# Kernel tuning notes

Hardware: AMD Instinct MI355X
Metric: run time of the kernel (lower is better)

The kernel has to match this reference:

```python
import jax, jax.numpy as jnp
import numpy as np

CON_SIZE = 1024  # num_gz; used in the 1/sqrt(con_size) score scaling


def setup_inputs() -> dict:
    key = jax.random.key(0)
    k1, k2, k3, k4, k5 = jax.random.split(key, 5)
    B, K, D, P = 1024, 256, 1024, 768
    return {
        "joint_feature": jax.random.normal(k1, (B, D), dtype=jnp.float32),
        "confounder_dictionary": jax.random.normal(k2, (K, D), dtype=jnp.float32),
        "prior": jax.random.uniform(k3, (K, 1), dtype=jnp.float32),
        "Wq": jax.random.normal(k4, (D, P), dtype=jnp.float32) * (1.0 / np.sqrt(D)),
        "Wk": jax.random.normal(k5, (D, P), dtype=jnp.float32) * (1.0 / np.sqrt(D)),
    }


def reference(joint_feature, confounder_dictionary, prior, Wq, Wk):
    # dot_product_intervention
    q = joint_feature @ Wq                       # [B, 768]
    k = confounder_dictionary @ Wk               # [K, 768]
    scores = (q @ k.T) * (1.0 / jnp.sqrt(jnp.float32(CON_SIZE)))  # [B, K]
    attn = jax.nn.softmax(scores, axis=-1)       # softmax over confounders
    # (attn[b,k,1] * conf[k,d] * prior[k,1]).sum(1)  == attn @ (conf * prior)
    g_z = jnp.einsum('bk,kd->bd', attn, confounder_dictionary * prior)  # [B, D]
    return joint_feature + g_z
```

## Files before the change

### kernel.cpp

```cpp
#include <hip/hip_runtime.h>
#include <hip/hip_bf16.h>


typedef __attribute__((ext_vector_type(8))) short short8;
typedef __attribute__((ext_vector_type(4))) float f32x4;

__device__ __forceinline__ ushort f2bf(float x) {
    union { float f; uint u; } c; c.f = x;
    return (ushort)((c.u + 0x7FFFu + ((c.u >> 16) & 1u)) >> 16);
}
__device__ __forceinline__ float bflo(uint u) {
    union { uint u; float f; } c; c.u = u << 16; return c.f;
}
__device__ __forceinline__ float bfhi(uint u) {
    union { uint u; float f; } c; c.u = u & 0xFFFF0000u; return c.f;
}

__global__ __launch_bounds__(256)
void prep_kernel(const float* __restrict__ J, const float* __restrict__ conf,
                 const float* __restrict__ prior, const float* __restrict__ Wq,
                 const float* __restrict__ Wk,
                 ushort* __restrict__ Jb, ushort* __restrict__ confb,
                 ushort* __restrict__ WqT, ushort* __restrict__ WkT,
                 ushort* __restrict__ cpT)
{
    const int t = threadIdx.x;
    int b = blockIdx.x;

    if (b < 1280) {
        const float* src; ushort* dst; int base;
        if (b < 1024) { src = J;    dst = Jb;    base = b * 1024; }
        else          { src = conf; dst = confb; base = (b - 1024) * 1024; }
        const float4 v = *(const float4*)(src + base + t * 4);
        ushort4 o;
        o.x = f2bf(v.x); o.y = f2bf(v.y); o.z = f2bf(v.z); o.w = f2bf(v.w);
        *(ushort4*)(dst + base + t * 4) = o;
        return;
    }

    __shared__ float tile[32][33];
    const float* src; ushort* dst; int R, C, tpr; bool usePrior;
    if (b < 2048)      { b -= 1280; src = Wq;   dst = WqT; R = 1024; C = 768;  tpr = 24; usePrior = false; }
    else if (b < 2816) { b -= 2048; src = Wk;   dst = WkT; R = 1024; C = 768;  tpr = 24; usePrior = false; }
    else               { b -= 2816; src = conf; dst = cpT; R = 256;  C = 1024; tpr = 32; usePrior = true;  }
    const int rt = b / tpr, ct = b % tpr;

    {
        const int row = t >> 3, c4 = (t & 7) << 2;
        const float4 v = *(const float4*)(src + (size_t)(rt * 32 + row) * C + ct * 32 + c4);
        const float p = usePrior ? prior[rt * 32 + row] : 1.0f;
        tile[row][c4 + 0] = v.x * p; tile[row][c4 + 1] = v.y * p;
        tile[row][c4 + 2] = v.z * p; tile[row][c4 + 3] = v.w * p;
    }
    __syncthreads();
    {
        const int orow = t >> 3, oc4 = (t & 7) << 2;
        ushort4 o;
        o.x = f2bf(tile[oc4 + 0][orow]); o.y = f2bf(tile[oc4 + 1][orow]);
        o.z = f2bf(tile[oc4 + 2][orow]); o.w = f2bf(tile[oc4 + 3][orow]);
        *(ushort4*)(dst + (size_t)(ct * 32 + orow) * R + rt * 32 + oc4) = o;
    }
}

struct LdsTiles {
    __align__(16) ushort As[64][72];
    __align__(16) ushort Bs[64][72];
};

__device__ __forceinline__
void gemm64_core(LdsTiles& S, const ushort* __restrict__ A,
                 const ushort* __restrict__ B, ushort* __restrict__ Cb,
                 int m0, int n0, int N, int K, float scale)
{
    const int t = threadIdx.x;
    const int wave = t >> 6, lane = t & 63;
    const int wm = (wave >> 1) * 32, wn = (wave & 1) * 32;
    const int lrow = lane & 15, lko = (lane >> 4) * 8;

    f32x4 acc[2][2];
    #pragma unroll
    for (int i = 0; i < 2; ++i)
        #pragma unroll
        for (int j = 0; j < 2; ++j) acc[i][j] = (f32x4)0.0f;

    const int sr = t >> 2, sk = (t & 3) << 4;
    const ushort* Ap = A + (size_t)(m0 + sr) * K + sk;
    const ushort* Bp = B + (size_t)(n0 + sr) * K + sk;

    uint4 av0 = *(const uint4*)(Ap);
    uint4 av1 = *(const uint4*)(Ap + 8);
    uint4 bv0 = *(const uint4*)(Bp);
    uint4 bv1 = *(const uint4*)(Bp + 8);

    for (int k0 = 0; k0 < K; k0 += 64) {
        *(uint4*)&S.As[sr][sk]     = av0;
        *(uint4*)&S.As[sr][sk + 8] = av1;
        *(uint4*)&S.Bs[sr][sk]     = bv0;
        *(uint4*)&S.Bs[sr][sk + 8] = bv1;
        __syncthreads();
        if (k0 + 64 < K) {
            av0 = *(const uint4*)(Ap + k0 + 64);
            av1 = *(const uint4*)(Ap + k0 + 72);
            bv0 = *(const uint4*)(Bp + k0 + 64);
            bv1 = *(const uint4*)(Bp + k0 + 72);
        }
        #pragma unroll
        for (int kk = 0; kk < 64; kk += 32) {
            const short8 a0 = *(const short8*)&S.As[wm + lrow][kk + lko];
            const short8 a1 = *(const short8*)&S.As[wm + 16 + lrow][kk + lko];
            const short8 b0 = *(const short8*)&S.Bs[wn + lrow][kk + lko];
            const short8 b1 = *(const short8*)&S.Bs[wn + 16 + lrow][kk + lko];
            acc[0][0] = __builtin_amdgcn_mfma_f32_16x16x32_bf16(a0, b0, acc[0][0], 0, 0, 0);
            acc[0][1] = __builtin_amdgcn_mfma_f32_16x16x32_bf16(a0, b1, acc[0][1], 0, 0, 0);
            acc[1][0] = __builtin_amdgcn_mfma_f32_16x16x32_bf16(a1, b0, acc[1][0], 0, 0, 0);
            acc[1][1] = __builtin_amdgcn_mfma_f32_16x16x32_bf16(a1, b1, acc[1][1], 0, 0, 0);
        }
        __syncthreads();
    }

    const int quad = lane >> 4;
    #pragma unroll
    for (int i = 0; i < 2; ++i)
        #pragma unroll
        for (int j = 0; j < 2; ++j)
            #pragma unroll
            for (int r = 0; r < 4; ++r) {
                const int m = m0 + wm + i * 16 + quad * 4 + r;
                const int n = n0 + wn + j * 16 + lrow;
                Cb[(size_t)m * N + n] = f2bf(acc[i][j][r] * scale);
            }
}

__global__ __launch_bounds__(256)
void qk_kernel(const ushort* __restrict__ Jb, const ushort* __restrict__ WqT,
               const ushort* __restrict__ confb, const ushort* __restrict__ WkT,
               ushort* __restrict__ qb, ushort* __restrict__ kmb)
{
    __shared__ LdsTiles S;
    int bid = blockIdx.x;
    const ushort *A, *B; ushort* C;
    if (bid < 192) { A = Jb; B = WqT; C = qb; }
    else           { bid -= 192; A = confb; B = WkT; C = kmb; }
    const int mt = bid / 12, nt = bid % 12;
    gemm64_core(S, A, B, C, mt * 64, nt * 64, 768, 1024, 1.0f);
}

__global__ __launch_bounds__(256)
void scores_kernel(const ushort* __restrict__ qb, const ushort* __restrict__ kmb,
                   ushort* __restrict__ sc)
{
    __shared__ LdsTiles S;
    gemm64_core(S, qb, kmb, sc, blockIdx.y * 64, blockIdx.x * 64, 256, 768, 0.03125f);
}

__global__ __launch_bounds__(256)
void out_kernel(const ushort* __restrict__ sc, const ushort* __restrict__ cpT,
                const float* __restrict__ J, float* __restrict__ out)
{
    __shared__ __align__(16) ushort At[64][264];
    __shared__ __align__(16) ushort Bs[64][72];
    __shared__ float rowInv[64];

    const int t = threadIdx.x;
    const int m0 = blockIdx.y * 64, n0 = blockIdx.x * 64;

    {
        const int row = t >> 2;
        const int cb  = (t & 3) * 64;
        const ushort* srow = sc + (size_t)(m0 + row) * 256 + cb;
        uint4 s[8];
        #pragma unroll
        for (int i = 0; i < 8; ++i) s[i] = *(const uint4*)(srow + i * 8);

        float mx = -1e30f;
        #pragma unroll
        for (int i = 0; i < 8; ++i) {
            mx = fmaxf(mx, fmaxf(fmaxf(bflo(s[i].x), bfhi(s[i].x)),
                                 fmaxf(bflo(s[i].y), bfhi(s[i].y))));
            mx = fmaxf(mx, fmaxf(fmaxf(bflo(s[i].z), bfhi(s[i].z)),
                                 fmaxf(bflo(s[i].w), bfhi(s[i].w))));
        }
        mx = fmaxf(mx, __shfl_xor(mx, 1));
        mx = fmaxf(mx, __shfl_xor(mx, 2));

        float sum = 0.0f;
        #pragma unroll
        for (int i = 0; i < 8; ++i) {
            uint4 o;
            uint* su = (uint*)&s[i];
            uint* ou = (uint*)&o;
            #pragma unroll
            for (int w = 0; w < 4; ++w) {
                const ushort e0 = f2bf(__expf(bflo(su[w]) - mx));
                const ushort e1 = f2bf(__expf(bfhi(su[w]) - mx));
                sum += bflo((uint)e0) + bflo((uint)e1);
                ou[w] = (uint)e0 | ((uint)e1 << 16);
            }
            *(uint4*)&At[row][cb + i * 8] = o;
        }
        sum += __shfl_xor(sum, 1);
        sum += __shfl_xor(sum, 2);
        if ((t & 3) == 0) rowInv[row] = 1.0f / sum;
    }
    __syncthreads();

    const int wave = t >> 6, lane = t & 63;
    const int wm = (wave >> 1) * 32, wn = (wave & 1) * 32;
    const int lrow = lane & 15, lko = (lane >> 4) * 8;

    f32x4 acc[2][2];
    #pragma unroll
    for (int i = 0; i < 2; ++i)
        #pragma unroll
        for (int j = 0; j < 2; ++j) acc[i][j] = (f32x4)0.0f;

    const int sr = t >> 2, sk = (t & 3) << 4;
    const ushort* Bp = cpT + (size_t)(n0 + sr) * 256 + sk;
    uint4 bv0 = *(const uint4*)(Bp);
    uint4 bv1 = *(const uint4*)(Bp + 8);

    for (int k0 = 0; k0 < 256; k0 += 64) {
        *(uint4*)&Bs[sr][sk]     = bv0;
        *(uint4*)&Bs[sr][sk + 8] = bv1;
        __syncthreads();
        if (k0 + 64 < 256) {
            bv0 = *(const uint4*)(Bp + k0 + 64);
            bv1 = *(const uint4*)(Bp + k0 + 72);
        }
        #pragma unroll
        for (int kk = 0; kk < 64; kk += 32) {
            const short8 a0 = *(const short8*)&At[wm + lrow][k0 + kk + lko];
            const short8 a1 = *(const short8*)&At[wm + 16 + lrow][k0 + kk + lko];
            const short8 b0 = *(const short8*)&Bs[wn + lrow][kk + lko];
            const short8 b1 = *(const short8*)&Bs[wn + 16 + lrow][kk + lko];
            acc[0][0] = __builtin_amdgcn_mfma_f32_16x16x32_bf16(a0, b0, acc[0][0], 0, 0, 0);
            acc[0][1] = __builtin_amdgcn_mfma_f32_16x16x32_bf16(a0, b1, acc[0][1], 0, 0, 0);
            acc[1][0] = __builtin_amdgcn_mfma_f32_16x16x32_bf16(a1, b0, acc[1][0], 0, 0, 0);
            acc[1][1] = __builtin_amdgcn_mfma_f32_16x16x32_bf16(a1, b1, acc[1][1], 0, 0, 0);
        }
        __syncthreads();
    }

    const int quad = lane >> 4;
    #pragma unroll
    for (int i = 0; i < 2; ++i)
        #pragma unroll
        for (int j = 0; j < 2; ++j)
            #pragma unroll
            for (int r = 0; r < 4; ++r) {
                const int mrel = wm + i * 16 + quad * 4 + r;
                const int m = m0 + mrel;
                const int n = n0 + wn + j * 16 + lrow;
                const size_t off = (size_t)m * 1024 + n;
                out[off] = acc[i][j][r] * rowInv[mrel] + J[off];
            }
}

extern "C" void kernel_launch(void* const* d_in, const int* in_sizes, int n_in,
                              void* d_out, int out_size, void* d_ws, size_t ws_size,
                              hipStream_t stream)
{
    const float* J     = (const float*)d_in[0];
    const float* conf  = (const float*)d_in[1];
    const float* prior = (const float*)d_in[2];
    const float* Wq    = (const float*)d_in[3];
    const float* Wk    = (const float*)d_in[4];
    float* out = (float*)d_out;

    ushort* ws = (ushort*)d_ws;
    ushort* Jb    = ws;
    ushort* confb = Jb    + 1048576;
    ushort* WqT   = confb + 262144;
    ushort* WkT   = WqT   + 786432;
    ushort* cpT   = WkT   + 786432;
    ushort* qb    = cpT   + 262144;
    ushort* kmb   = qb    + 786432;
    ushort* scb   = kmb   + 196608;

    prep_kernel<<<3072, 256, 0, stream>>>(J, conf, prior, Wq, Wk,
                                          Jb, confb, WqT, WkT, cpT);
    qk_kernel<<<240, 256, 0, stream>>>(Jb, WqT, confb, WkT, qb, kmb);
    scores_kernel<<<dim3(4, 16), 256, 0, stream>>>(qb, kmb, scb);
    out_kernel<<<dim3(16, 16), 256, 0, stream>>>(scb, cpT, J, out);
}
```

Measured before the change: 95.80 us.

## Fuse four kernel launches into one cooperative persistent kernel with grid syncs

Merges the prep, QK projection, scores and softmax-output kernels into a single cooperative launch of 256 blocks, separated by grid-wide barriers. Prep work is redistributed as grid-stride loops over the same blocks. Shared memory is unified through a union. The aim is to remove per-launch overhead and inter-kernel gaps. The cost is that the prep phase now runs with far fewer blocks, and the scores phase uses only 64 of 256 blocks, so load balance and parallelism drop within phases.

Result: slower. 195.9 us (+104.5%).

```diff
diff --git a/kernel.cpp b/kernel.cpp
--- a/kernel.cpp
+++ b/kernel.cpp
@@ -1,5 +1,8 @@
 #include <hip/hip_runtime.h>
 #include <hip/hip_bf16.h>
+#include <hip/hip_cooperative_groups.h>
+
+namespace cg = cooperative_groups;
 
 
 typedef __attribute__((ext_vector_type(8))) short short8;
@@ -16,59 +19,23 @@
     union { uint u; float f; } c; c.u = u & 0xFFFF0000u; return c.f;
 }
 
-__global__ __launch_bounds__(256)
-void prep_kernel(const float* __restrict__ J, const float* __restrict__ conf,
-                 const float* __restrict__ prior, const float* __restrict__ Wq,
-                 const float* __restrict__ Wk,
-                 ushort* __restrict__ Jb, ushort* __restrict__ confb,
-                 ushort* __restrict__ WqT, ushort* __restrict__ WkT,
-                 ushort* __restrict__ cpT)
-{
-    const int t = threadIdx.x;
-    int b = blockIdx.x;
-
-    if (b < 1280) {
-        const float* src; ushort* dst; int base;
-        if (b < 1024) { src = J;    dst = Jb;    base = b * 1024; }
-        else          { src = conf; dst = confb; base = (b - 1024) * 1024; }
-        const float4 v = *(const float4*)(src + base + t * 4);
-        ushort4 o;
-        o.x = f2bf(v.x); o.y = f2bf(v.y); o.z = f2bf(v.z); o.w = f2bf(v.w);
-        *(ushort4*)(dst + base + t * 4) = o;
-        return;
-    }
-
-    __shared__ float tile[32][33];
-    const float* src; ushort* dst; int R, C, tpr; bool usePrior;
-    if (b < 2048)      { b -= 1280; src = Wq;   dst = WqT; R = 1024; C = 768;  tpr = 24; usePrior = false; }
-    else if (b < 2816) { b -= 2048; src = Wk;   dst = WkT; R = 1024; C = 768;  tpr = 24; usePrior = false; }
-    else               { b -= 2816; src = conf; dst = cpT; R = 256;  C = 1024; tpr = 32; usePrior = true;  }
-    const int rt = b / tpr, ct = b % tpr;
-
-    {
-        const int row = t >> 3, c4 = (t & 7) << 2;
-        const float4 v = *(const float4*)(src + (size_t)(rt * 32 + row) * C + ct * 32 + c4);
-        const float p = usePrior ? prior[rt * 32 + row] : 1.0f;
-        tile[row][c4 + 0] = v.x * p; tile[row][c4 + 1] = v.y * p;
-        tile[row][c4 + 2] = v.z * p; tile[row][c4 + 3] = v.w * p;
-    }
-    __syncthreads();
-    {
-        const int orow = t >> 3, oc4 = (t & 7) << 2;
-        ushort4 o;
-        o.x = f2bf(tile[oc4 + 0][orow]); o.y = f2bf(tile[oc4 + 1][orow]);
-        o.z = f2bf(tile[oc4 + 2][orow]); o.w = f2bf(tile[oc4 + 3][orow]);
-        *(ushort4*)(dst + (size_t)(ct * 32 + orow) * R + rt * 32 + oc4) = o;
-    }
-}
-
-struct LdsTiles {
+struct GemmTiles {
     __align__(16) ushort As[64][72];
     __align__(16) ushort Bs[64][72];
 };
+struct OutTiles {
+    __align__(16) ushort At[64][264];
+    __align__(16) ushort Bs[64][72];
+    float rowInv[64];
+};
+union SharedU {
+    float     tr[32][33];
+    GemmTiles g;
+    OutTiles  o;
+};
 
 __device__ __forceinline__
-void gemm64_core(LdsTiles& S, const ushort* __restrict__ A,
+void gemm64_core(GemmTiles& S, const ushort* __restrict__ A,
                  const ushort* __restrict__ B, ushort* __restrict__ Cb,
                  int m0, int n0, int N, int K, float scale)
 {
@@ -132,128 +99,165 @@
 }
 
 __global__ __launch_bounds__(256)
-void qk_kernel(const ushort* __restrict__ Jb, const ushort* __restrict__ WqT,
-               const ushort* __restrict__ confb, const ushort* __restrict__ WkT,
-               ushort* __restrict__ qb, ushort* __restrict__ kmb)
+void ccim_fused(const float* __restrict__ J, const float* __restrict__ conf,
+                const float* __restrict__ prior, const float* __restrict__ Wq,
+                const float* __restrict__ Wk,
+                ushort* __restrict__ Jb, ushort* __restrict__ confb,
+                ushort* __restrict__ WqT, ushort* __restrict__ WkT,
+                ushort* __restrict__ cpT, ushort* __restrict__ qb,
+                ushort* __restrict__ kmb, ushort* __restrict__ scb,
+                float* __restrict__ out)
 {
-    __shared__ LdsTiles S;
-    int bid = blockIdx.x;
-    const ushort *A, *B; ushort* C;
-    if (bid < 192) { A = Jb; B = WqT; C = qb; }
-    else           { bid -= 192; A = confb; B = WkT; C = kmb; }
-    const int mt = bid / 12, nt = bid % 12;
-    gemm64_core(S, A, B, C, mt * 64, nt * 64, 768, 1024, 1.0f);
-}
-
-__global__ __launch_bounds__(256)
-void scores_kernel(const ushort* __restrict__ qb, const ushort* __restrict__ kmb,
-                   ushort* __restrict__ sc)
-{
-    __shared__ LdsTiles S;
-    gemm64_core(S, qb, kmb, sc, blockIdx.y * 64, blockIdx.x * 64, 256, 768, 0.03125f);
-}
-
-__global__ __launch_bounds__(256)
-void out_kernel(const ushort* __restrict__ sc, const ushort* __restrict__ cpT,
-                const float* __restrict__ J, float* __restrict__ out)
-{
-    __shared__ __align__(16) ushort At[64][264];
-    __shared__ __align__(16) ushort Bs[64][72];
-    __shared__ float rowInv[64];
-
+    __shared__ SharedU S;
     const int t = threadIdx.x;
-    const int m0 = blockIdx.y * 64, n0 = blockIdx.x * 64;
+    const int bid = blockIdx.x;
+    cg::grid_group grid = cg::this_grid();
 
     {
-        const int row = t >> 2;
-        const int cb  = (t & 3) * 64;
-        const ushort* srow = sc + (size_t)(m0 + row) * 256 + cb;
-        uint4 s[8];
-        #pragma unroll
-        for (int i = 0; i < 8; ++i) s[i] = *(const uint4*)(srow + i * 8);
-
-        float mx = -1e30f;
-        #pragma unroll
-        for (int i = 0; i < 8; ++i) {
-            mx = fmaxf(mx, fmaxf(fmaxf(bflo(s[i].x), bfhi(s[i].x)),
-                                 fmaxf(bflo(s[i].y), bfhi(s[i].y))));
-            mx = fmaxf(mx, fmaxf(fmaxf(bflo(s[i].z), bfhi(s[i].z)),
-                                 fmaxf(bflo(s[i].w), bfhi(s[i].w))));
-        }
-        mx = fmaxf(mx, __shfl_xor(mx, 1));
-        mx = fmaxf(mx, __shfl_xor(mx, 2));
-
-        float sum = 0.0f;
-        #pragma unroll
-        for (int i = 0; i < 8; ++i) {
-            uint4 o;
-            uint* su = (uint*)&s[i];
-            uint* ou = (uint*)&o;
-            #pragma unroll
-            for (int w = 0; w < 4; ++w) {
-                const ushort e0 = f2bf(__expf(bflo(su[w]) - mx));
-                const ushort e1 = f2bf(__expf(bfhi(su[w]) - mx));
-                sum += bflo((uint)e0) + bflo((uint)e1);
-                ou[w] = (uint)e0 | ((uint)e1 << 16);
-            }
-            *(uint4*)&At[row][cb + i * 8] = o;
-        }
-        sum += __shfl_xor(sum, 1);
-        sum += __shfl_xor(sum, 2);
-        if ((t & 3) == 0) rowInv[row] = 1.0f / sum;
-    }
-    __syncthreads();
-
-    const int wave = t >> 6, lane = t & 63;
-    const int wm = (wave >> 1) * 32, wn = (wave & 1) * 32;
-    const int lrow = lane & 15, lko = (lane >> 4) * 8;
-
-    f32x4 acc[2][2];
-    #pragma unroll
-    for (int i = 0; i < 2; ++i)
-        #pragma unroll
-        for (int j = 0; j < 2; ++j) acc[i][j] = (f32x4)0.0f;
-
-    const int sr = t >> 2, sk = (t & 3) << 4;
-    const ushort* Bp = cpT + (size_t)(n0 + sr) * 256 + sk;
-    uint4 bv0 = *(const uint4*)(Bp);
-    uint4 bv1 = *(const uint4*)(Bp + 8);
-
-    for (int k0 = 0; k0 < 256; k0 += 64) {
-        *(uint4*)&Bs[sr][sk]     = bv0;
-        *(uint4*)&Bs[sr][sk + 8] = bv1;
+        const int gtid = bid * 256 + t;
+        #pragma unroll 1
+        for (int u = gtid; u < 327680; u += 65536) {
+            const float* src; ushort* dst; int e;
+            if (u < 262144) { src = J;    dst = Jb;    e = u * 4; }
+            else            { src = conf; dst = confb; e = (u - 262144) * 4; }
+            const float4 v = *(const float4*)(src + e);
+            ushort4 o;
+            o.x = f2bf(v.x); o.y = f2bf(v.y); o.z = f2bf(v.z); o.w = f2bf(v.w);
+            *(ushort4*)(dst + e) = o;
+        }
+        #pragma unroll 1
+        for (int tb = bid; tb < 1792; tb += 256) {
+            const float* src; ushort* dst; int R, C, rt, ct; bool useP;
+            if (tb < 768)       { src = Wq;   dst = WqT; R = 1024; C = 768;  rt = tb / 24;          ct = tb % 24;          useP = false; }
+            else if (tb < 1536) { const int b2 = tb - 768;  src = Wk;   dst = WkT; R = 1024; C = 768;  rt = b2 / 24; ct = b2 % 24; useP = false; }
+            else                { const int b2 = tb - 1536; src = conf; dst = cpT; R = 256;  C = 1024; rt = b2 / 32; ct = b2 % 32; useP = true;  }
+            {
+                const int row = t >> 3, c4 = (t & 7) << 2;
+                const float4 v = *(const float4*)(src + (size_t)(rt * 32 + row) * C + ct * 32 + c4);
+                const float p = useP ? prior[rt * 32 + row] : 1.0f;
+                S.tr[row][c4 + 0] = v.x * p; S.tr[row][c4 + 1] = v.y * p;
+                S.tr[row][c4 + 2] = v.z * p; S.tr[row][c4 + 3] = v.w * p;
+            }
+            __syncthreads();
+            {
+                const int orow = t >> 3, oc4 = (t & 7) << 2;
+                ushort4 o;
+                o.x = f2bf(S.tr[oc4 + 0][orow]); o.y = f2bf(S.tr[oc4 + 1][orow]);
+                o.z = f2bf(S.tr[oc4 + 2][orow]); o.w = f2bf(S.tr[oc4 + 3][orow]);
+                *(ushort4*)(dst + (size_t)(ct * 32 + orow) * R + rt * 32 + oc4) = o;
+            }
+            __syncthreads();
+        }
+    }
+    grid.sync();
+
+    if (bid < 240) {
+        const ushort *A, *B; ushort* C; int b2 = bid;
+        if (b2 < 192) { A = Jb; B = WqT; C = qb; }
+        else          { b2 -= 192; A = confb; B = WkT; C = kmb; }
+        gemm64_core(S.g, A, B, C, (b2 / 12) * 64, (b2 % 12) * 64, 768, 1024, 1.0f);
+    }
+    grid.sync();
+
+    if (bid < 64) {
+        gemm64_core(S.g, qb, kmb, scb, (bid >> 2) * 64, (bid & 3) * 64, 256, 768, 0.03125f);
+    }
+    grid.sync();
+
+    {
+        const int m0 = (bid >> 4) * 64, n0 = (bid & 15) * 64;
+
+        {
+            const int row = t >> 2;
+            const int cb  = (t & 3) * 64;
+            const ushort* srow = scb + (size_t)(m0 + row) * 256 + cb;
+            uint4 s[8];
+            #pragma unroll
+            for (int i = 0; i < 8; ++i) s[i] = *(const uint4*)(srow + i * 8);
+
+            float mx = -1e30f;
+            #pragma unroll
+            for (int i = 0; i < 8; ++i) {
+                mx = fmaxf(mx, fmaxf(fmaxf(bflo(s[i].x), bfhi(s[i].x)),
+                                     fmaxf(bflo(s[i].y), bfhi(s[i].y))));
+                mx = fmaxf(mx, fmaxf(fmaxf(bflo(s[i].z), bfhi(s[i].z)),
+                                     fmaxf(bflo(s[i].w), bfhi(s[i].w))));
+            }
+            mx = fmaxf(mx, __shfl_xor(mx, 1));
+            mx = fmaxf(mx, __shfl_xor(mx, 2));
+
+            float sum = 0.0f;
+            #pragma unroll
+            for (int i = 0; i < 8; ++i) {
+                uint4 o;
+                uint* su = (uint*)&s[i];
+                uint* ou = (uint*)&o;
+                #pragma unroll
+                for (int w = 0; w < 4; ++w) {
+                    const ushort e0 = f2bf(__expf(bflo(su[w]) - mx));
+                    const ushort e1 = f2bf(__expf(bfhi(su[w]) - mx));
+                    sum += bflo((uint)e0) + bflo((uint)e1);
+                    ou[w] = (uint)e0 | ((uint)e1 << 16);
+                }
+                *(uint4*)&S.o.At[row][cb + i * 8] = o;
+            }
+            sum += __shfl_xor(sum, 1);
+            sum += __shfl_xor(sum, 2);
+            if ((t & 3) == 0) S.o.rowInv[row] = 1.0f / sum;
+        }
         __syncthreads();
-        if (k0 + 64 < 256) {
-            bv0 = *(const uint4*)(Bp + k0 + 64);
-            bv1 = *(const uint4*)(Bp + k0 + 72);
-        }
-        #pragma unroll
-        for (int kk = 0; kk < 64; kk += 32) {
-            const short8 a0 = *(const short8*)&At[wm + lrow][k0 + kk + lko];
-            const short8 a1 = *(const short8*)&At[wm + 16 + lrow][k0 + kk + lko];
-            const short8 b0 = *(const short8*)&Bs[wn + lrow][kk + lko];
-            const short8 b1 = *(const short8*)&Bs[wn + 16 + lrow][kk + lko];
-            acc[0][0] = __builtin_amdgcn_mfma_f32_16x16x32_bf16(a0, b0, acc[0][0], 0, 0, 0);
-            acc[0][1] = __builtin_amdgcn_mfma_f32_16x16x32_bf16(a0, b1, acc[0][1], 0, 0, 0);
-            acc[1][0] = __builtin_amdgcn_mfma_f32_16x16x32_bf16(a1, b0, acc[1][0], 0, 0, 0);
-            acc[1][1] = __builtin_amdgcn_mfma_f32_16x16x32_bf16(a1, b1, acc[1][1], 0, 0, 0);
-        }
-        __syncthreads();
-    }
-
-    const int quad = lane >> 4;
-    #pragma unroll
-    for (int i = 0; i < 2; ++i)
-        #pragma unroll
-        for (int j = 0; j < 2; ++j)
-            #pragma unroll
-            for (int r = 0; r < 4; ++r) {
-                const int mrel = wm + i * 16 + quad * 4 + r;
-                const int m = m0 + mrel;
-                const int n = n0 + wn + j * 16 + lrow;
-                const size_t off = (size_t)m * 1024 + n;
-                out[off] = acc[i][j][r] * rowInv[mrel] + J[off];
-            }
+
+        const int wave = t >> 6, lane = t & 63;
+        const int wm = (wave >> 1) * 32, wn = (wave & 1) * 32;
+        const int lrow = lane & 15, lko = (lane >> 4) * 8;
+
+        f32x4 acc[2][2];
+        #pragma unroll
+        for (int i = 0; i < 2; ++i)
+            #pragma unroll
+            for (int j = 0; j < 2; ++j) acc[i][j] = (f32x4)0.0f;
+
+        const int sr = t >> 2, sk = (t & 3) << 4;
+        const ushort* Bp = cpT + (size_t)(n0 + sr) * 256 + sk;
+        uint4 bv0 = *(const uint4*)(Bp);
+        uint4 bv1 = *(const uint4*)(Bp + 8);
+
+        for (int k0 = 0; k0 < 256; k0 += 64) {
+            *(uint4*)&S.o.Bs[sr][sk]     = bv0;
+            *(uint4*)&S.o.Bs[sr][sk + 8] = bv1;
+            __syncthreads();
+            if (k0 + 64 < 256) {
+                bv0 = *(const uint4*)(Bp + k0 + 64);
+                bv1 = *(const uint4*)(Bp + k0 + 72);
+            }
+            #pragma unroll
+            for (int kk = 0; kk < 64; kk += 32) {
+                const short8 a0 = *(const short8*)&S.o.At[wm + lrow][k0 + kk + lko];
+                const short8 a1 = *(const short8*)&S.o.At[wm + 16 + lrow][k0 + kk + lko];
+                const short8 b0 = *(const short8*)&S.o.Bs[wn + lrow][kk + lko];
+                const short8 b1 = *(const short8*)&S.o.Bs[wn + 16 + lrow][kk + lko];
+                acc[0][0] = __builtin_amdgcn_mfma_f32_16x16x32_bf16(a0, b0, acc[0][0], 0, 0, 0);
+                acc[0][1] = __builtin_amdgcn_mfma_f32_16x16x32_bf16(a0, b1, acc[0][1], 0, 0, 0);
+                acc[1][0] = __builtin_amdgcn_mfma_f32_16x16x32_bf16(a1, b0, acc[1][0], 0, 0, 0);
+                acc[1][1] = __builtin_amdgcn_mfma_f32_16x16x32_bf16(a1, b1, acc[1][1], 0, 0, 0);
+            }
+            __syncthreads();
+        }
+
+        const int quad = lane >> 4;
+        #pragma unroll
+        for (int i = 0; i < 2; ++i)
+            #pragma unroll
+            for (int j = 0; j < 2; ++j)
+                #pragma unroll
+                for (int r = 0; r < 4; ++r) {
+                    const int mrel = wm + i * 16 + quad * 4 + r;
+                    const int m = m0 + mrel;
+                    const int n = n0 + wn + j * 16 + lrow;
+                    const size_t off = (size_t)m * 1024 + n;
+                    out[off] = acc[i][j][r] * S.o.rowInv[mrel] + J[off];
+                }
+    }
 }
 
 extern "C" void kernel_launch(void* const* d_in, const int* in_sizes, int n_in,
@@ -277,9 +281,8 @@
     ushort* kmb   = qb    + 786432;
     ushort* scb   = kmb   + 196608;
 
-    prep_kernel<<<3072, 256, 0, stream>>>(J, conf, prior, Wq, Wk,
-                                          Jb, confb, WqT, WkT, cpT);
-    qk_kernel<<<240, 256, 0, stream>>>(Jb, WqT, confb, WkT, qb, kmb);
-    scores_kernel<<<dim3(4, 16), 256, 0, stream>>>(qb, kmb, scb);
-    out_kernel<<<dim3(16, 16), 256, 0, stream>>>(scb, cpT, J, out);
-}
+    void* args[] = { &J, &conf, &prior, &Wq, &Wk,
+                     &Jb, &confb, &WqT, &WkT, &cpT, &qb, &kmb, &scb, &out };
+    hipLaunchCooperativeKernel((void*)ccim_fused, dim3(256), dim3(256),
+                               args, 0, stream);
+}
```
